# Performance work log

Measured on AMD Instinct MI355X. Metric: run time of the kernel, lower is better.

## Reference

```python
import math
import jax, jax.numpy as jnp
import numpy as np

B, T, H, A, F = 2, 2048, 2048, 2048, 8192
L, LID, EPS = 24, 0, 1e-5
NEG_INF = -1e38


def setup_inputs() -> dict:
    key = jax.random.key(0)
    ks = jax.random.split(key, 8)
    s = 0.02
    # RWKV init-derived time parameters for layer_id=0, num_hidden_layers=24
    ratio_0_to_1 = LID / (L - 1)          # 0.0
    ratio_1_to_almost_0 = 1.0 - LID / L    # 1.0
    x = jnp.arange(H, dtype=jnp.float32) / H
    tmk = jnp.power(x, ratio_1_to_almost_0)
    tmv = tmk + 0.3 * ratio_0_to_1
    tmr = jnp.power(x, 0.5 * ratio_1_to_almost_0)
    zigzag = 0.5 * (jnp.arange(1, A + 1, dtype=jnp.float32) % 3 - 1)
    time_first = jnp.full((A,), math.log(0.3), dtype=jnp.float32) + zigzag
    h = jnp.arange(A, dtype=jnp.float32)
    time_decay = -5.0 + 8.0 * (h / (A - 1)) ** (0.7 + 1.3 * ratio_0_to_1)
    return {
        'hidden': jax.random.normal(ks[0], (B, T, H), jnp.float32),
        'pre_w': jnp.ones((H,), jnp.float32), 'pre_b': jnp.zeros((H,), jnp.float32),
        'ln1_w': jnp.ones((H,), jnp.float32), 'ln1_b': jnp.zeros((H,), jnp.float32),
        'ln2_w': jnp.ones((H,), jnp.float32), 'ln2_b': jnp.zeros((H,), jnp.float32),
        'time_decay': time_decay, 'time_first': time_first,
        'tmk': tmk, 'tmv': tmv, 'tmr': tmr,
        'Wk': jax.random.normal(ks[1], (H, A), jnp.float32) * s,
        'Wv': jax.random.normal(ks[2], (H, A), jnp.float32) * s,
        'Wr': jax.random.normal(ks[3], (H, A), jnp.float32) * s,
        'Wo': jax.random.normal(ks[4], (A, H), jnp.float32) * s,
        'f_tmk': jnp.power(x, ratio_1_to_almost_0), 'f_tmr': jnp.power(x, ratio_1_to_almost_0),
        'f_Wk': jax.random.normal(ks[5], (H, F), jnp.float32) * s,
        'f_Wr': jax.random.normal(ks[6], (H, H), jnp.float32) * s,
        'f_Wv': jax.random.normal(ks[7], (F, H), jnp.float32) * s,
    }


def _ln(x, w, b):
    mu = x.mean(-1, keepdims=True)
    var = ((x - mu) ** 2).mean(-1, keepdims=True)
    return (x - mu) * jax.lax.rsqrt(var + EPS) * w + b


def _token_shift(x):
    # sx state is zeros at init: prepend a zero row, drop the last token
    return jnp.concatenate((jnp.zeros_like(x[:, :1, :]), x[:, :-1, :]), axis=1)


def _forward(hidden, pre_w, pre_b, ln1_w, ln1_b, ln2_w, ln2_b,
             time_decay, time_first, tmk, tmv, tmr, Wk, Wv, Wr, Wo,
             f_tmk, f_tmr, f_Wk, f_Wr, f_Wv):
    h0 = _ln(hidden, pre_w, pre_b)          # pre_ln (layer_id == 0)
    # ---- time mixing (RwkvSelfAttention) ----
    x1 = _ln(h0, ln1_w, ln1_b)
    cx = _token_shift(x1)
    kx = x1 * tmk + cx * (1 - tmk)
    vx = x1 * tmv + cx * (1 - tmv)
    rx = x1 * tmr + cx * (1 - tmr)
    r = jax.nn.sigmoid(rx @ Wr)             # [B,T,A]
    k = kx @ Wk
    v = vx @ Wv
    w_decay = -jnp.exp(time_decay)          # [A]

    def step(carry, kv):
        aa, bb, pp = carry                  # each [B,A]
        kk, vv = kv                         # each [B,A]
        ww = time_first + kk
        q = jnp.maximum(pp, ww)
        e1 = jnp.exp(pp - q)
        e2 = jnp.exp(ww - q)
        out = (e1 * aa + e2 * vv) / (e1 * bb + e2)
        ww2 = w_decay + pp
        q2 = jnp.maximum(ww2, kk)
        e1 = jnp.exp(ww2 - q2)
        e2 = jnp.exp(kk - q2)
        return (e1 * aa + e2 * vv, e1 * bb + e2, q2), out

    init = (jnp.zeros((B, A), k.dtype), jnp.zeros((B, A), k.dtype),
            jnp.full((B, A), NEG_INF, jnp.float32))
    _, wkv = jax.lax.scan(step, init, (jnp.swapaxes(k, 0, 1), jnp.swapaxes(v, 0, 1)))
    wkv = jnp.swapaxes(wkv, 0, 1)           # [B,T,A]
    h1 = h0 + (r * wkv) @ Wo
    # ---- channel mixing (RwkvFeedForward) ----
    x2 = _ln(h1, ln2_w, ln2_b)
    cx2 = _token_shift(x2)
    kx2 = x2 * f_tmk + cx2 * (1 - f_tmk)
    rx2 = x2 * f_tmr + cx2 * (1 - f_tmr)
    r2 = jax.nn.sigmoid(rx2 @ f_Wr)
    kk2 = jnp.square(jax.nn.relu(kx2 @ f_Wk))
    return h1 + r2 * (kk2 @ f_Wv)


def reference(hidden, pre_w, pre_b, ln1_w, ln1_b, ln2_w, ln2_b,
              time_decay, time_first, tmk, tmv, tmr, Wk, Wv, Wr, Wo,
              f_tmk, f_tmr, f_Wk, f_Wr, f_Wv):
    return _forward(hidden, pre_w, pre_b, ln1_w, ln1_b, ln2_w, ln2_b,
                    time_decay, time_first, tmk, tmv, tmr, Wk, Wv, Wr, Wo,
                    f_tmk, f_tmr, f_Wk, f_Wr, f_Wv)
```

## Files before the change

### kernel.cpp

```cpp
#include <hip/hip_runtime.h>

#define B_  2
#define T_  2048
#define H_  2048
#define A_  2048
#define F_  8192
#define BT_ 4096

typedef __bf16  bf16x8 __attribute__((ext_vector_type(8)));
typedef float   f32x4  __attribute__((ext_vector_type(4)));
typedef short   short8 __attribute__((ext_vector_type(8)));

__device__ __forceinline__ float bf2f(unsigned short b) {
  return __uint_as_float(((unsigned)b) << 16);
}
__device__ __forceinline__ unsigned short f2bf(float f) {
  unsigned u = __float_as_uint(f);
  unsigned r = (u + 0x7FFFu + ((u >> 16) & 1u)) >> 16;
  return (unsigned short)r;
}

typedef __attribute__((address_space(3))) void lds_void_t;
typedef __attribute__((address_space(1))) const void gc_void_t;
__device__ __forceinline__ void gload_lds16(const void* g, void* l) {
  __builtin_amdgcn_global_load_lds((gc_void_t*)g, (lds_void_t*)l, 16, 0, 0);
}

__global__ void canary_kernel(float* out) { out[threadIdx.x] = 1000.0f; }

__global__ __launch_bounds__(256) void transpose_bf16_kernel(
    const float* __restrict__ src, unsigned short* __restrict__ dst, int Kd, int Nd)
{
  __shared__ float tile[32][33];
  const int tx = threadIdx.x & 31;
  const int ty = threadIdx.x >> 5;
  const int n0 = blockIdx.x * 32;
  const int k0 = blockIdx.y * 32;
#pragma unroll
  for (int i = 0; i < 32; i += 8)
    tile[ty + i][tx] = src[(size_t)(k0 + ty + i) * Nd + n0 + tx];
  __syncthreads();
#pragma unroll
  for (int i = 0; i < 32; i += 8)
    dst[(size_t)(n0 + ty + i) * Kd + k0 + tx] = f2bf(tile[tx][ty + i]);
}

__device__ __forceinline__ void block_reduce2(float& a, float& b) {
#pragma unroll
  for (int off = 32; off > 0; off >>= 1) {
    a += __shfl_down(a, off, 64);
    b += __shfl_down(b, off, 64);
  }
  __shared__ float sa[4], sb[4];
  const int lane = threadIdx.x & 63, w = threadIdx.x >> 6;
  __syncthreads();
  if (lane == 0) { sa[w] = a; sb[w] = b; }
  __syncthreads();
  a = sa[0] + sa[1] + sa[2] + sa[3];
  b = sb[0] + sb[1] + sb[2] + sb[3];
}

__global__ __launch_bounds__(256) void ln_pre_kernel(
    const float* __restrict__ hidden,
    const float* __restrict__ pw, const float* __restrict__ pb,
    const float* __restrict__ w1, const float* __restrict__ b1,
    float* __restrict__ h0, unsigned short* __restrict__ x1)
{
  const int row = blockIdx.x, tid = threadIdx.x;
  const int c0 = tid * 8;
  const size_t base = (size_t)row * H_ + c0;
  float x[8];
  float4 v0 = *(const float4*)(hidden + base);
  float4 v1 = *(const float4*)(hidden + base + 4);
  x[0]=v0.x; x[1]=v0.y; x[2]=v0.z; x[3]=v0.w;
  x[4]=v1.x; x[5]=v1.y; x[6]=v1.z; x[7]=v1.w;
  float s = 0.f, s2 = 0.f;
#pragma unroll
  for (int j = 0; j < 8; ++j) { s += x[j]; s2 += x[j]*x[j]; }
  block_reduce2(s, s2);
  float mu  = s * (1.f / H_);
  float inv = rsqrtf(fmaxf(s2 * (1.f / H_) - mu*mu, 0.f) + 1e-5f);
  float y[8];
#pragma unroll
  for (int j = 0; j < 8; ++j) y[j] = (x[j] - mu) * inv * pw[c0+j] + pb[c0+j];
  *(float4*)(h0 + base)     = make_float4(y[0],y[1],y[2],y[3]);
  *(float4*)(h0 + base + 4) = make_float4(y[4],y[5],y[6],y[7]);
  s = 0.f; s2 = 0.f;
#pragma unroll
  for (int j = 0; j < 8; ++j) { s += y[j]; s2 += y[j]*y[j]; }
  block_reduce2(s, s2);
  mu  = s * (1.f / H_);
  inv = rsqrtf(fmaxf(s2 * (1.f / H_) - mu*mu, 0.f) + 1e-5f);
  unsigned o[4];
#pragma unroll
  for (int p = 0; p < 4; ++p) {
    unsigned lo = f2bf((y[2*p]   - mu) * inv * w1[c0+2*p]   + b1[c0+2*p]);
    unsigned hi = f2bf((y[2*p+1] - mu) * inv * w1[c0+2*p+1] + b1[c0+2*p+1]);
    o[p] = lo | (hi << 16);
  }
  *(uint4*)(x1 + base) = make_uint4(o[0], o[1], o[2], o[3]);
}

__global__ __launch_bounds__(256) void lnmix2_kernel(
    const float* __restrict__ h1,
    const float* __restrict__ w_, const float* __restrict__ b_,
    const float* __restrict__ tmk_, const float* __restrict__ tmr_,
    unsigned short* __restrict__ kx2b, unsigned short* __restrict__ rx2b)
{
  const int row = blockIdx.x, tid = threadIdx.x;
  const int t = row & (T_ - 1);
  const int c0 = tid * 8;
  const size_t base = (size_t)row * H_ + c0;
  float x[8], p[8];
  {
    float4 v0 = *(const float4*)(h1 + base);
    float4 v1 = *(const float4*)(h1 + base + 4);
    x[0]=v0.x; x[1]=v0.y; x[2]=v0.z; x[3]=v0.w;
    x[4]=v1.x; x[5]=v1.y; x[6]=v1.z; x[7]=v1.w;
  }
  const bool hasp = (t > 0);
  if (hasp) {
    float4 v0 = *(const float4*)(h1 + base - H_);
    float4 v1 = *(const float4*)(h1 + base - H_ + 4);
    p[0]=v0.x; p[1]=v0.y; p[2]=v0.z; p[3]=v0.w;
    p[4]=v1.x; p[5]=v1.y; p[6]=v1.z; p[7]=v1.w;
  } else {
#pragma unroll
    for (int j = 0; j < 8; ++j) p[j] = 0.f;
  }
  float s = 0.f, s2 = 0.f;
#pragma unroll
  for (int j = 0; j < 8; ++j) { s += x[j]; s2 += x[j]*x[j]; }
  block_reduce2(s, s2);
  const float mu  = s * (1.f / H_);
  const float inv = rsqrtf(fmaxf(s2 * (1.f / H_) - mu*mu, 0.f) + 1e-5f);
  float sp = 0.f, sp2 = 0.f;
#pragma unroll
  for (int j = 0; j < 8; ++j) { sp += p[j]; sp2 += p[j]*p[j]; }
  block_reduce2(sp, sp2);
  const float mup  = sp * (1.f / H_);
  const float invp = rsqrtf(fmaxf(sp2 * (1.f / H_) - mup*mup, 0.f) + 1e-5f);
  unsigned ok[4], orr[4];
#pragma unroll
  for (int q = 0; q < 4; ++q) {
    unsigned ko = 0, ro = 0;
#pragma unroll
    for (int h = 0; h < 2; ++h) {
      const int j = q*2 + h;
      const float xr = (x[j] - mu) * inv * w_[c0+j] + b_[c0+j];
      const float cr = hasp ? (p[j] - mup) * invp * w_[c0+j] + b_[c0+j] : 0.f;
      ko |= (unsigned)f2bf(fmaf(xr - cr, tmk_[c0+j], cr)) << (h*16);
      ro |= (unsigned)f2bf(fmaf(xr - cr, tmr_[c0+j], cr)) << (h*16);
    }
    ok[q] = ko; orr[q] = ro;
  }
  *(uint4*)(kx2b + base) = make_uint4(ok[0],ok[1],ok[2],ok[3]);
  *(uint4*)(rx2b + base) = make_uint4(orr[0],orr[1],orr[2],orr[3]);
}

__global__ __launch_bounds__(256) void mix1_kernel(
    const unsigned short* __restrict__ x,
    const float* __restrict__ tm_,
    unsigned short* __restrict__ outb)
{
  const int row = blockIdx.x;
  const int t = row & (T_ - 1);
  const int c0 = threadIdx.x * 8;
  const size_t base = (size_t)row * H_ + c0;
  uint4 xv = *(const uint4*)(x + base);
  uint4 cv = make_uint4(0u,0u,0u,0u);
  if (t > 0) cv = *(const uint4*)(x + base - H_);
  const unsigned xs[4] = {xv.x, xv.y, xv.z, xv.w};
  const unsigned cs[4] = {cv.x, cv.y, cv.z, cv.w};
  unsigned oo[4];
#pragma unroll
  for (int p = 0; p < 4; ++p) {
    unsigned w = 0;
#pragma unroll
    for (int h = 0; h < 2; ++h) {
      const int j = p*2 + h;
      float xf = bf2f((unsigned short)((xs[p] >> (h*16)) & 0xFFFFu));
      float cf = bf2f((unsigned short)((cs[p] >> (h*16)) & 0xFFFFu));
      w |= (unsigned)f2bf(fmaf(xf - cf, tm_[c0+j], cf)) << (h*16);
    }
    oo[p] = w;
  }
  *(uint4*)(outb + base) = make_uint4(oo[0],oo[1],oo[2],oo[3]);
}

#define WKV_G 32
#define WKV_C 32
#define WKV_L 64

__global__ __launch_bounds__(1024) void wkv_scan_kernel(
    const unsigned short* __restrict__ kg, const unsigned short* __restrict__ vg,
    const unsigned short* __restrict__ rg,
    const float* __restrict__ time_first, const float* __restrict__ time_decay,
    unsigned short* __restrict__ rwkv)
{
  const int tid = threadIdx.x;
  const int al  = tid & (WKV_G - 1);
  const int c   = tid >> 5;
  const int b   = blockIdx.x >> 6;
  const int ag  = blockIdx.x & 63;
  const int a   = ag * WKV_G + al;
  const float tf = time_first[a];
  const float w  = -__expf(time_decay[a]);
  const size_t cb = (size_t)b * T_ * A_ + a + (size_t)c * WKV_L * A_;

  float aa = 0.f, bb = 0.f, pp = -1e38f;
  {
    float kb[4], vb[4];
#pragma unroll
    for (int j = 0; j < 4; ++j) {
      kb[j] = bf2f(kg[cb + (size_t)j * A_]);
      vb[j] = bf2f(vg[cb + (size_t)j * A_]);
    }
    for (int t0 = 0; t0 < WKV_L; t0 += 4) {
#pragma unroll
      for (int j = 0; j < 4; ++j) {
        const float kk = kb[j], vv = vb[j];
        const int tn = t0 + j + 4;
        if (tn < WKV_L) {
          kb[j] = bf2f(kg[cb + (size_t)tn * A_]);
          vb[j] = bf2f(vg[cb + (size_t)tn * A_]);
        }
        float ww2 = w + pp;
        float q2  = fmaxf(ww2, kk);
        float e1  = __expf(ww2 - q2);
        float e2  = __expf(kk  - q2);
        aa = e1*aa + e2*vv;
        bb = e1*bb + e2;
        pp = q2;
      }
    }
  }
  __shared__ float saa[WKV_C][WKV_G], sbb[WKV_C][WKV_G], spp[WKV_C][WKV_G];
  saa[c][al] = aa; sbb[c][al] = bb; spp[c][al] = pp;
  __syncthreads();

  if (tid < WKV_G) {
    float Aa = 0.f, Bb = 0.f, Pp = -1e38f;
    const float Lw = (float)WKV_L * w;
    for (int cc = 0; cc < WKV_C; ++cc) {
      const float na = saa[cc][tid], nb = sbb[cc][tid], np = spp[cc][tid];
      saa[cc][tid] = Aa; sbb[cc][tid] = Bb; spp[cc][tid] = Pp;
      const float p1 = Pp + Lw;
      const float pc = fmaxf(p1, np);
      const float f1 = __expf(p1 - pc);
      const float f2 = __expf(np - pc);
      Aa = f1*Aa + f2*na;
      Bb = f1*Bb + f2*nb;
      Pp = pc;
    }
  }
  __syncthreads();
  aa = saa[c][al]; bb = sbb[c][al]; pp = spp[c][al];

  {
    float kb[4], vb[4], rb[4];
#pragma unroll
    for (int j = 0; j < 4; ++j) {
      kb[j] = bf2f(kg[cb + (size_t)j * A_]);
      vb[j] = bf2f(vg[cb + (size_t)j * A_]);
      rb[j] = bf2f(rg[cb + (size_t)j * A_]);
    }
    for (int t0 = 0; t0 < WKV_L; t0 += 4) {
#pragma unroll
      for (int j = 0; j < 4; ++j) {
        const float kk = kb[j], vv = vb[j], rr = rb[j];
        const int tn = t0 + j + 4;
        if (tn < WKV_L) {
          kb[j] = bf2f(kg[cb + (size_t)tn * A_]);
          vb[j] = bf2f(vg[cb + (size_t)tn * A_]);
          rb[j] = bf2f(rg[cb + (size_t)tn * A_]);
        }
        float ww = tf + kk;
        float q  = fmaxf(pp, ww);
        float e1 = __expf(pp - q);
        float e2 = __expf(ww - q);
        float o  = (e1*aa + e2*vv) / (e1*bb + e2);
        float sr = 1.f / (1.f + __expf(-rr));
        rwkv[cb + (size_t)(t0 + j) * A_] = f2bf(sr * o);
        float ww2 = w + pp;
        float q2  = fmaxf(ww2, kk);
        e1 = __expf(ww2 - q2);
        e2 = __expf(kk  - q2);
        aa = e1*aa + e2*vv;
        bb = e1*bb + e2;
        pp = q2;
      }
    }
  }
}

enum { EPI_BF16 = 0, EPI_ADDIP = 1, EPI_RELU2 = 2, EPI_SIGADD = 3 };

template <int BM, int NBUF, int RG, int CG, int EPI>
__global__ __launch_bounds__(512) void gemm4_kernel(
    const unsigned short* __restrict__ Ap, const unsigned short* __restrict__ Bp,
    void* __restrict__ Cp, int K, int Nn,
    const unsigned short* __restrict__ sigb)
{
  constexpr int BN = 256;
  constexpr int FM = BM / 32;
  constexpr int FN = 4;
  __shared__ unsigned short As[NBUF * BM * 64];
  __shared__ unsigned short Bs[NBUF * BN * 64];
  const int tid  = threadIdx.x;
  const int lane = tid & 63;
  const int lr = lane & 15;
  const int hi = lane >> 4;
  const int rx7 = lr & 7;
  const int wid = tid >> 6;
  const int wm = wid >> 2, wn = wid & 3;
  const int rowW = wm * (BM / 2);
  const int colW = wn * 64;
  const int gx = gridDim.x;
  const int gy = gridDim.y;
  const int flat = blockIdx.y * gx + blockIdx.x;
  const int xcd = flat & 7;
  const int j = flat >> 3;
  const int rgc = gy / RG;
  const int r_idx = xcd % rgc;
  const int c_idx = xcd / rgc;
  const int row_l = j % RG;
  const int col_l = j / RG;
  const long row0 = (long)(r_idx * RG + row_l) * BM;
  const long col0 = (long)(c_idx * CG + col_l) * BN;
  const unsigned short* Ab = Ap + (size_t)row0 * K;
  const unsigned short* Bb = Bp + (size_t)col0 * K;
  const int srow8 = tid >> 3;
  const int sslot = (tid & 7) ^ (srow8 & 7);
  f32x4 acc[FM][FN] = {};

  auto SP0 = [&](int bufi, int tt) {
    unsigned short* asb = As + bufi * (BM * 64);
    unsigned short* bsb = Bs + bufi * (BN * 64);
    const size_t ko = (size_t)tt * 64 + sslot * 8;
    gload_lds16(Ab + (size_t)srow8        * K + ko, asb + tid * 8);
    gload_lds16(Ab + (size_t)(srow8 + 64) * K + ko, asb + 4096 + tid * 8);
    gload_lds16(Bb + (size_t)srow8        * K + ko, bsb + tid * 8);
  };
  auto SP1 = [&](int bufi, int tt) {
    unsigned short* bsb = Bs + bufi * (BN * 64);
    const size_t ko = (size_t)tt * 64 + sslot * 8;
    gload_lds16(Bb + (size_t)(srow8 + 64)  * K + ko, bsb + 4096  + tid * 8);
    gload_lds16(Bb + (size_t)(srow8 + 128) * K + ko, bsb + 8192  + tid * 8);
    gload_lds16(Bb + (size_t)(srow8 + 192) * K + ko, bsb + 12288 + tid * 8);
  };
  auto SPq = [&](int bufi, int tt, int q) {
    const size_t ko = (size_t)tt * 64 + sslot * 8;
    if (q < 2) {
      unsigned short* asb = As + bufi * (BM * 64);
      gload_lds16(Ab + (size_t)(srow8 + q*128)      * K + ko, asb + q*8192 + tid * 8);
      gload_lds16(Ab + (size_t)(srow8 + q*128 + 64) * K + ko, asb + q*8192 + 4096 + tid * 8);
    } else {
      const int qq = q - 2;
      unsigned short* bsb = Bs + bufi * (BN * 64);
      gload_lds16(Bb + (size_t)(srow8 + qq*128)      * K + ko, bsb + qq*8192 + tid * 8);
      gload_lds16(Bb + (size_t)(srow8 + qq*128 + 64) * K + ko, bsb + qq*8192 + 4096 + tid * 8);
    }
  };

  const int nt = K >> 6;
  if constexpr (BM == 128) {
    SP0(0, 0); SP1(0, 0);
    if constexpr (NBUF == 3) { SP0(1, 1); SP1(1, 1); }
  } else {
#pragma unroll
    for (int q = 0; q < 4; ++q) SPq(0, 0, q);
  }
  int cur = 0;
  for (int t = 0; t < nt; ++t) {
    if constexpr (NBUF == 3) {
      if (t + 1 < nt) asm volatile("s_waitcnt vmcnt(6)" ::: "memory");
      else            asm volatile("s_waitcnt vmcnt(0)" ::: "memory");
    } else {
      asm volatile("s_waitcnt vmcnt(0)" ::: "memory");
    }
    __builtin_amdgcn_s_barrier();
    int nb = cur + (NBUF - 1); if (nb >= NBUF) nb -= NBUF;
    const unsigned short* asb = As + cur * (BM * 64);
    const unsigned short* bsb = Bs + cur * (BN * 64);
    if constexpr (BM == 128) {
#pragma unroll
      for (int kk = 0; kk < 2; ++kk) {
        bf16x8 af[4], bfr[4];
#pragma unroll
        for (int m = 0; m < 4; ++m) {
          const int row = rowW + m*16 + lr;
          const int ps = (kk*4 + hi) ^ rx7;
          af[m] = __builtin_bit_cast(bf16x8, *(const short8*)(asb + row*64 + ps*8));
        }
#pragma unroll
        for (int n = 0; n < 4; ++n) {
          const int row = colW + n*16 + lr;
          const int ps = (kk*4 + hi) ^ rx7;
          bfr[n] = __builtin_bit_cast(bf16x8, *(const short8*)(bsb + row*64 + ps*8));
        }
        if (t + NBUF - 1 < nt) { if (kk == 0) SP0(nb, t + NBUF - 1); else SP1(nb, t + NBUF - 1); }
        asm volatile("s_waitcnt lgkmcnt(0)" ::: "memory");
        __builtin_amdgcn_sched_barrier(0);
        __builtin_amdgcn_s_setprio(1);
#pragma unroll
        for (int m = 0; m < 4; ++m)
#pragma unroll
          for (int n = 0; n < 4; ++n)
            acc[m][n] = __builtin_amdgcn_mfma_f32_16x16x32_bf16(af[m], bfr[n], acc[m][n], 0, 0, 0);
        __builtin_amdgcn_s_setprio(0);
      }
    } else {
      bf16x8 bfrk[4];
#pragma unroll
      for (int sub = 0; sub < 4; ++sub) {
        const int kk = sub >> 1, mh = sub & 1;
        bf16x8 af[4];
#pragma unroll
        for (int m = 0; m < 4; ++m) {
          const int row = rowW + (mh*4 + m)*16 + lr;
          const int ps = (kk*4 + hi) ^ rx7;
          af[m] = __builtin_bit_cast(bf16x8, *(const short8*)(asb + row*64 + ps*8));
        }
        if (mh == 0) {
#pragma unroll
          for (int n = 0; n < 4; ++n) {
            const int row = colW + n*16 + lr;
            const int ps = (kk*4 + hi) ^ rx7;
            bfrk[n] = __builtin_bit_cast(bf16x8, *(const short8*)(bsb + row*64 + ps*8));
          }
        }
        if (t + 1 < nt) SPq(nb, t + 1, sub);
        asm volatile("s_waitcnt lgkmcnt(0)" ::: "memory");
        __builtin_amdgcn_sched_barrier(0);
        __builtin_amdgcn_s_setprio(1);
#pragma unroll
        for (int m = 0; m < 4; ++m)
#pragma unroll
          for (int n = 0; n < 4; ++n)
            acc[mh*4 + m][n] = __builtin_amdgcn_mfma_f32_16x16x32_bf16(af[m], bfrk[n], acc[mh*4 + m][n], 0, 0, 0);
        __builtin_amdgcn_s_setprio(0);
      }
    }
    cur = (cur + 1 == NBUF) ? 0 : cur + 1;
  }

#pragma unroll
  for (int m = 0; m < FM; ++m) {
#pragma unroll
    for (int n = 0; n < FN; ++n) {
      const long col = col0 + colW + n*16 + lr;
#pragma unroll
      for (int j2 = 0; j2 < 4; ++j2) {
        const long row = row0 + rowW + m*16 + hi*4 + j2;
        const size_t idx = (size_t)row * Nn + col;
        const float v = acc[m][n][j2];
        if (EPI == EPI_BF16) {
          ((unsigned short*)Cp)[idx] = f2bf(v);
        } else if (EPI == EPI_ADDIP) {
          float* C = (float*)Cp;
          C[idx] = C[idx] + v;
        } else if (EPI == EPI_RELU2) {
          float rr = v > 0.f ? v : 0.f;
          ((unsigned short*)Cp)[idx] = f2bf(rr * rr);
        } else {
          float s = 1.f / (1.f + __expf(-bf2f(sigb[idx])));
          float* C = (float*)Cp;
          C[idx] = C[idx] + s * v;
        }
      }
    }
  }
}

#define MB(x) ((size_t)(x) << 20)
#define WS_NEED MB(184)

extern "C" void kernel_launch(void* const* d_in, const int* in_sizes, int n_in,
                              void* d_out, int out_size, void* d_ws, size_t ws_size,
                              hipStream_t stream) {
  const float* hidden     = (const float*)d_in[0];
  const float* pre_w      = (const float*)d_in[1];
  const float* pre_b      = (const float*)d_in[2];
  const float* ln1_w      = (const float*)d_in[3];
  const float* ln1_b      = (const float*)d_in[4];
  const float* ln2_w      = (const float*)d_in[5];
  const float* ln2_b      = (const float*)d_in[6];
  const float* time_decay = (const float*)d_in[7];
  const float* time_first = (const float*)d_in[8];
  const float* tmk        = (const float*)d_in[9];
  const float* tmv        = (const float*)d_in[10];
  const float* tmr        = (const float*)d_in[11];
  const float* Wk         = (const float*)d_in[12];
  const float* Wv         = (const float*)d_in[13];
  const float* Wr         = (const float*)d_in[14];
  const float* Wo         = (const float*)d_in[15];
  const float* f_tmk      = (const float*)d_in[16];
  const float* f_tmr      = (const float*)d_in[17];
  const float* f_Wk       = (const float*)d_in[18];
  const float* f_Wr       = (const float*)d_in[19];
  const float* f_Wv       = (const float*)d_in[20];
  float* out = (float*)d_out;
  char*  ws  = (char*)d_ws;

  if (ws_size < WS_NEED) {
    canary_kernel<<<1, 256, 0, stream>>>(out);
    return;
  }

  unsigned short* fWkT = (unsigned short*)(ws + MB(0));
  unsigned short* fWvT = (unsigned short*)(ws + MB(32));
  unsigned short* WkT  = (unsigned short*)(ws + MB(64));
  unsigned short* WvT  = (unsigned short*)(ws + MB(72));
  unsigned short* WrT  = (unsigned short*)(ws + MB(80));
  unsigned short* WoT  = (unsigned short*)(ws + MB(88));
  unsigned short* fWrT = (unsigned short*)(ws + MB(96));
  unsigned short* KK   = (unsigned short*)(ws + MB(64));
  unsigned short* S1   = (unsigned short*)(ws + MB(104));
  unsigned short* S4   = (unsigned short*)(ws + MB(120));
  unsigned short* S2   = (unsigned short*)(ws + MB(136));
  unsigned short* S3   = (unsigned short*)(ws + MB(152));
  unsigned short* M1   = (unsigned short*)(ws + MB(168));

  const dim3 blk(256);
  const dim3 blk512(512);
  const dim3 gSmall(8, 32);
  const dim3 gRelu(32, 16);

  transpose_bf16_kernel<<<dim3(64, 64),  blk, 0, stream>>>(Wk,   WkT,  2048, 2048);
  transpose_bf16_kernel<<<dim3(64, 64),  blk, 0, stream>>>(Wv,   WvT,  2048, 2048);
  transpose_bf16_kernel<<<dim3(64, 64),  blk, 0, stream>>>(Wr,   WrT,  2048, 2048);
  transpose_bf16_kernel<<<dim3(64, 64),  blk, 0, stream>>>(Wo,   WoT,  2048, 2048);
  transpose_bf16_kernel<<<dim3(64, 64),  blk, 0, stream>>>(f_Wr, fWrT, 2048, 2048);
  transpose_bf16_kernel<<<dim3(256, 64), blk, 0, stream>>>(f_Wk, fWkT, 2048, 8192);
  transpose_bf16_kernel<<<dim3(64, 256), blk, 0, stream>>>(f_Wv, fWvT, 8192, 2048);

  ln_pre_kernel<<<BT_, blk, 0, stream>>>(hidden, pre_w, pre_b, ln1_w, ln1_b, out, S1);

  mix1_kernel<<<BT_, blk, 0, stream>>>(S1, tmk, M1);
  gemm4_kernel<128,3,8,4,EPI_BF16><<<gSmall, blk512, 0, stream>>>(M1, WkT, S2, 2048, 2048, nullptr);
  mix1_kernel<<<BT_, blk, 0, stream>>>(S1, tmv, M1);
  gemm4_kernel<128,3,8,4,EPI_BF16><<<gSmall, blk512, 0, stream>>>(M1, WvT, S3, 2048, 2048, nullptr);
  mix1_kernel<<<BT_, blk, 0, stream>>>(S1, tmr, M1);
  gemm4_kernel<128,3,8,4,EPI_BF16><<<gSmall, blk512, 0, stream>>>(M1, WrT, S4, 2048, 2048, nullptr);

  wkv_scan_kernel<<<dim3(128), dim3(1024), 0, stream>>>(S2, S3, S4, time_first, time_decay, S1);

  gemm4_kernel<128,3,8,4,EPI_ADDIP><<<gSmall, blk512, 0, stream>>>(S1, WoT, out, 2048, 2048, nullptr);

  lnmix2_kernel<<<BT_, blk, 0, stream>>>(out, ln2_w, ln2_b, f_tmk, f_tmr, M1, S2);

  gemm4_kernel<128,3,8,4,EPI_BF16><<<gSmall, blk512, 0, stream>>>(S2, fWrT, S3, 2048, 2048, nullptr);

  gemm4_kernel<256,2,8,8,EPI_RELU2><<<gRelu, blk512, 0, stream>>>(M1, fWkT, KK, 2048, 8192, nullptr);

  gemm4_kernel<128,3,8,4,EPI_SIGADD><<<gSmall, blk512, 0, stream>>>(KK, fWvT, out, 8192, 2048, S3);
}
```

Baseline: 703.6 us.

## Rework GEMM pipeline into double-buffered K-half stages with finer-grained prefetch

Replaces the 3-buffer (and 2-buffer for BM=256) GEMM mainloop with a double buffer. Each 64-wide K tile is split into two 32-wide halves, each with its own barrier and prefetch slot. The LDS layout changes to 32-element rows with a 4-way XOR swizzle. This cuts LDS use, which may allow more occupancy, and aims to overlap loads at half-tile granularity. It adds an extra barrier per tile and a different bank-conflict pattern.

```diff
diff --git a/kernel.cpp b/kernel.cpp
--- a/kernel.cpp
+++ b/kernel.cpp
@@ -296,8 +296,8 @@
 
 enum { EPI_BF16 = 0, EPI_ADDIP = 1, EPI_RELU2 = 2, EPI_SIGADD = 3 };
 
-template <int BM, int NBUF, int RG, int CG, int EPI>
-__global__ __launch_bounds__(512) void gemm4_kernel(
+template <int BM, int RG, int CG, int EPI>
+__global__ __launch_bounds__(512) void gemm5_kernel(
     const unsigned short* __restrict__ Ap, const unsigned short* __restrict__ Bp,
     void* __restrict__ Cp, int K, int Nn,
     const unsigned short* __restrict__ sigb)
@@ -305,13 +305,13 @@
   constexpr int BN = 256;
   constexpr int FM = BM / 32;
   constexpr int FN = 4;
-  __shared__ unsigned short As[NBUF * BM * 64];
-  __shared__ unsigned short Bs[NBUF * BN * 64];
+  __shared__ unsigned short As[2 * BM * 64];
+  __shared__ unsigned short Bs[2 * BN * 64];
   const int tid  = threadIdx.x;
   const int lane = tid & 63;
   const int lr = lane & 15;
   const int hi = lane >> 4;
-  const int rx7 = lr & 7;
+  const int ps8 = (hi ^ (lr & 3)) * 8;
   const int wid = tid >> 6;
   const int wm = wid >> 2, wn = wid & 3;
   const int rowW = wm * (BM / 2);
@@ -330,107 +330,72 @@
   const long col0 = (long)(c_idx * CG + col_l) * BN;
   const unsigned short* Ab = Ap + (size_t)row0 * K;
   const unsigned short* Bb = Bp + (size_t)col0 * K;
-  const int srow8 = tid >> 3;
-  const int sslot = (tid & 7) ^ (srow8 & 7);
+  const int srow4 = tid >> 2;
+  const int sslot4 = (tid & 3) ^ (srow4 & 3);
   f32x4 acc[FM][FN] = {};
 
-  auto SP0 = [&](int bufi, int tt) {
-    unsigned short* asb = As + bufi * (BM * 64);
-    unsigned short* bsb = Bs + bufi * (BN * 64);
-    const size_t ko = (size_t)tt * 64 + sslot * 8;
-    gload_lds16(Ab + (size_t)srow8        * K + ko, asb + tid * 8);
-    gload_lds16(Ab + (size_t)(srow8 + 64) * K + ko, asb + 4096 + tid * 8);
-    gload_lds16(Bb + (size_t)srow8        * K + ko, bsb + tid * 8);
+  auto SP = [&](int bufi, int tt, int kh) {
+    const size_t ko = (size_t)tt * 64 + kh * 32 + sslot4 * 8;
+    unsigned short* asb = As + bufi * (BM * 64) + kh * (BM * 32);
+    unsigned short* bsb = Bs + bufi * (BN * 64) + kh * (BN * 32);
+    if constexpr (BM == 128) {
+      gload_lds16(Ab + (size_t)srow4 * K + ko, asb + tid * 8);
+    } else {
+      gload_lds16(Ab + (size_t)srow4         * K + ko, asb + tid * 8);
+      gload_lds16(Ab + (size_t)(srow4 + 128) * K + ko, asb + 4096 + tid * 8);
+    }
+    gload_lds16(Bb + (size_t)srow4         * K + ko, bsb + tid * 8);
+    gload_lds16(Bb + (size_t)(srow4 + 128) * K + ko, bsb + 4096 + tid * 8);
   };
-  auto SP1 = [&](int bufi, int tt) {
-    unsigned short* bsb = Bs + bufi * (BN * 64);
-    const size_t ko = (size_t)tt * 64 + sslot * 8;
-    gload_lds16(Bb + (size_t)(srow8 + 64)  * K + ko, bsb + 4096  + tid * 8);
-    gload_lds16(Bb + (size_t)(srow8 + 128) * K + ko, bsb + 8192  + tid * 8);
-    gload_lds16(Bb + (size_t)(srow8 + 192) * K + ko, bsb + 12288 + tid * 8);
-  };
-  auto SPq = [&](int bufi, int tt, int q) {
-    const size_t ko = (size_t)tt * 64 + sslot * 8;
-    if (q < 2) {
-      unsigned short* asb = As + bufi * (BM * 64);
-      gload_lds16(Ab + (size_t)(srow8 + q*128)      * K + ko, asb + q*8192 + tid * 8);
-      gload_lds16(Ab + (size_t)(srow8 + q*128 + 64) * K + ko, asb + q*8192 + 4096 + tid * 8);
-    } else {
-      const int qq = q - 2;
-      unsigned short* bsb = Bs + bufi * (BN * 64);
-      gload_lds16(Bb + (size_t)(srow8 + qq*128)      * K + ko, bsb + qq*8192 + tid * 8);
-      gload_lds16(Bb + (size_t)(srow8 + qq*128 + 64) * K + ko, bsb + qq*8192 + 4096 + tid * 8);
-    }
-  };
 
   const int nt = K >> 6;
-  if constexpr (BM == 128) {
-    SP0(0, 0); SP1(0, 0);
-    if constexpr (NBUF == 3) { SP0(1, 1); SP1(1, 1); }
-  } else {
-#pragma unroll
-    for (int q = 0; q < 4; ++q) SPq(0, 0, q);
-  }
-  int cur = 0;
+  SP(0, 0, 0); SP(0, 0, 1); SP(1, 1, 0);
   for (int t = 0; t < nt; ++t) {
-    if constexpr (NBUF == 3) {
-      if (t + 1 < nt) asm volatile("s_waitcnt vmcnt(6)" ::: "memory");
-      else            asm volatile("s_waitcnt vmcnt(0)" ::: "memory");
-    } else {
-      asm volatile("s_waitcnt vmcnt(0)" ::: "memory");
-    }
-    __builtin_amdgcn_s_barrier();
-    int nb = cur + (NBUF - 1); if (nb >= NBUF) nb -= NBUF;
+    const int cur = t & 1;
     const unsigned short* asb = As + cur * (BM * 64);
     const unsigned short* bsb = Bs + cur * (BN * 64);
+    const bool c1 = (t + 1 < nt);
     if constexpr (BM == 128) {
-#pragma unroll
-      for (int kk = 0; kk < 2; ++kk) {
-        bf16x8 af[4], bfr[4];
-#pragma unroll
-        for (int m = 0; m < 4; ++m) {
-          const int row = rowW + m*16 + lr;
-          const int ps = (kk*4 + hi) ^ rx7;
-          af[m] = __builtin_bit_cast(bf16x8, *(const short8*)(asb + row*64 + ps*8));
-        }
-#pragma unroll
-        for (int n = 0; n < 4; ++n) {
-          const int row = colW + n*16 + lr;
-          const int ps = (kk*4 + hi) ^ rx7;
-          bfr[n] = __builtin_bit_cast(bf16x8, *(const short8*)(bsb + row*64 + ps*8));
-        }
-        if (t + NBUF - 1 < nt) { if (kk == 0) SP0(nb, t + NBUF - 1); else SP1(nb, t + NBUF - 1); }
-        asm volatile("s_waitcnt lgkmcnt(0)" ::: "memory");
-        __builtin_amdgcn_sched_barrier(0);
-        __builtin_amdgcn_s_setprio(1);
-#pragma unroll
-        for (int m = 0; m < 4; ++m)
-#pragma unroll
-          for (int n = 0; n < 4; ++n)
-            acc[m][n] = __builtin_amdgcn_mfma_f32_16x16x32_bf16(af[m], bfr[n], acc[m][n], 0, 0, 0);
-        __builtin_amdgcn_s_setprio(0);
-      }
+      if (c1) asm volatile("s_waitcnt vmcnt(6)" ::: "memory");
+      else    asm volatile("s_waitcnt vmcnt(3)" ::: "memory");
+    } else {
+      if (c1) asm volatile("s_waitcnt vmcnt(8)" ::: "memory");
+      else    asm volatile("s_waitcnt vmcnt(4)" ::: "memory");
+    }
+    __builtin_amdgcn_s_barrier();
+    if (c1) SP((t + 1) & 1, t + 1, 1);
+    if constexpr (BM == 128) {
+      bf16x8 af[4], bfr[4];
+#pragma unroll
+      for (int m = 0; m < 4; ++m)
+        af[m] = __builtin_bit_cast(bf16x8,
+            *(const short8*)(asb + (rowW + m*16 + lr) * 32 + ps8));
+#pragma unroll
+      for (int n = 0; n < 4; ++n)
+        bfr[n] = __builtin_bit_cast(bf16x8,
+            *(const short8*)(bsb + (colW + n*16 + lr) * 32 + ps8));
+      asm volatile("s_waitcnt lgkmcnt(0)" ::: "memory");
+      __builtin_amdgcn_sched_barrier(0);
+      __builtin_amdgcn_s_setprio(1);
+#pragma unroll
+      for (int m = 0; m < 4; ++m)
+#pragma unroll
+        for (int n = 0; n < 4; ++n)
+          acc[m][n] = __builtin_amdgcn_mfma_f32_16x16x32_bf16(af[m], bfr[n], acc[m][n], 0, 0, 0);
+      __builtin_amdgcn_s_setprio(0);
     } else {
       bf16x8 bfrk[4];
 #pragma unroll
-      for (int sub = 0; sub < 4; ++sub) {
-        const int kk = sub >> 1, mh = sub & 1;
+      for (int n = 0; n < 4; ++n)
+        bfrk[n] = __builtin_bit_cast(bf16x8,
+            *(const short8*)(bsb + (colW + n*16 + lr) * 32 + ps8));
+#pragma unroll
+      for (int mh = 0; mh < 2; ++mh) {
         bf16x8 af[4];
 #pragma unroll
-        for (int m = 0; m < 4; ++m) {
-          const int row = rowW + (mh*4 + m)*16 + lr;
-          const int ps = (kk*4 + hi) ^ rx7;
-          af[m] = __builtin_bit_cast(bf16x8, *(const short8*)(asb + row*64 + ps*8));
-        }
-        if (mh == 0) {
-#pragma unroll
-          for (int n = 0; n < 4; ++n) {
-            const int row = colW + n*16 + lr;
-            const int ps = (kk*4 + hi) ^ rx7;
-            bfrk[n] = __builtin_bit_cast(bf16x8, *(const short8*)(bsb + row*64 + ps*8));
-          }
-        }
-        if (t + 1 < nt) SPq(nb, t + 1, sub);
+        for (int m = 0; m < 4; ++m)
+          af[m] = __builtin_bit_cast(bf16x8,
+              *(const short8*)(asb + (rowW + (mh*4 + m)*16 + lr) * 32 + ps8));
         asm volatile("s_waitcnt lgkmcnt(0)" ::: "memory");
         __builtin_amdgcn_sched_barrier(0);
         __builtin_amdgcn_s_setprio(1);
@@ -442,7 +407,62 @@
         __builtin_amdgcn_s_setprio(0);
       }
     }
-    cur = (cur + 1 == NBUF) ? 0 : cur + 1;
+    if constexpr (BM == 128) {
+      if (c1) asm volatile("s_waitcnt vmcnt(6)" ::: "memory");
+      else    asm volatile("s_waitcnt vmcnt(0)" ::: "memory");
+    } else {
+      if (c1) asm volatile("s_waitcnt vmcnt(8)" ::: "memory");
+      else    asm volatile("s_waitcnt vmcnt(0)" ::: "memory");
+    }
+    __builtin_amdgcn_s_barrier();
+    if (t + 2 < nt) SP(cur, t + 2, 0);
+    {
+      const unsigned short* asb1 = asb + BM * 32;
+      const unsigned short* bsb1 = bsb + BN * 32;
+      if constexpr (BM == 128) {
+        bf16x8 af[4], bfr[4];
+#pragma unroll
+        for (int m = 0; m < 4; ++m)
+          af[m] = __builtin_bit_cast(bf16x8,
+              *(const short8*)(asb1 + (rowW + m*16 + lr) * 32 + ps8));
+#pragma unroll
+        for (int n = 0; n < 4; ++n)
+          bfr[n] = __builtin_bit_cast(bf16x8,
+              *(const short8*)(bsb1 + (colW + n*16 + lr) * 32 + ps8));
+        asm volatile("s_waitcnt lgkmcnt(0)" ::: "memory");
+        __builtin_amdgcn_sched_barrier(0);
+        __builtin_amdgcn_s_setprio(1);
+#pragma unroll
+        for (int m = 0; m < 4; ++m)
+#pragma unroll
+          for (int n = 0; n < 4; ++n)
+            acc[m][n] = __builtin_amdgcn_mfma_f32_16x16x32_bf16(af[m], bfr[n], acc[m][n], 0, 0, 0);
+        __builtin_amdgcn_s_setprio(0);
+      } else {
+        bf16x8 bfrk[4];
+#pragma unroll
+        for (int n = 0; n < 4; ++n)
+          bfrk[n] = __builtin_bit_cast(bf16x8,
+              *(const short8*)(bsb1 + (colW + n*16 + lr) * 32 + ps8));
+#pragma unroll
+        for (int mh = 0; mh < 2; ++mh) {
+          bf16x8 af[4];
+#pragma unroll
+          for (int m = 0; m < 4; ++m)
+            af[m] = __builtin_bit_cast(bf16x8,
+                *(const short8*)(asb1 + (rowW + (mh*4 + m)*16 + lr) * 32 + ps8));
+          asm volatile("s_waitcnt lgkmcnt(0)" ::: "memory");
+          __builtin_amdgcn_sched_barrier(0);
+          __builtin_amdgcn_s_setprio(1);
+#pragma unroll
+          for (int m = 0; m < 4; ++m)
+#pragma unroll
+            for (int n = 0; n < 4; ++n)
+              acc[mh*4 + m][n] = __builtin_amdgcn_mfma_f32_16x16x32_bf16(af[m], bfrk[n], acc[mh*4 + m][n], 0, 0, 0);
+          __builtin_amdgcn_s_setprio(0);
+        }
+      }
+    }
   }
 
 #pragma unroll
@@ -538,21 +558,21 @@
   ln_pre_kernel<<<BT_, blk, 0, stream>>>(hidden, pre_w, pre_b, ln1_w, ln1_b, out, S1);
 
   mix1_kernel<<<BT_, blk, 0, stream>>>(S1, tmk, M1);
-  gemm4_kernel<128,3,8,4,EPI_BF16><<<gSmall, blk512, 0, stream>>>(M1, WkT, S2, 2048, 2048, nullptr);
+  gemm5_kernel<128,8,4,EPI_BF16><<<gSmall, blk512, 0, stream>>>(M1, WkT, S2, 2048, 2048, nullptr);
   mix1_kernel<<<BT_, blk, 0, stream>>>(S1, tmv, M1);
-  gemm4_kernel<128,3,8,4,EPI_BF16><<<gSmall, blk512, 0, stream>>>(M1, WvT, S3, 2048, 2048, nullptr);
+  gemm5_kernel<128,8,4,EPI_BF16><<<gSmall, blk512, 0, stream>>>(M1, WvT, S3, 2048, 2048, nullptr);
   mix1_kernel<<<BT_, blk, 0, stream>>>(S1, tmr, M1);
-  gemm4_kernel<128,3,8,4,EPI_BF16><<<gSmall, blk512, 0, stream>>>(M1, WrT, S4, 2048, 2048, nullptr);
+  gemm5_kernel<128,8,4,EPI_BF16><<<gSmall, blk512, 0, stream>>>(M1, WrT, S4, 2048, 2048, nullptr);
 
   wkv_scan_kernel<<<dim3(128), dim3(1024), 0, stream>>>(S2, S3, S4, time_first, time_decay, S1);
 
-  gemm4_kernel<128,3,8,4,EPI_ADDIP><<<gSmall, blk512, 0, stream>>>(S1, WoT, out, 2048, 2048, nullptr);
+  gemm5_kernel<128,8,4,EPI_ADDIP><<<gSmall, blk512, 0, stream>>>(S1, WoT, out, 2048, 2048, nullptr);
 
   lnmix2_kernel<<<BT_, blk, 0, stream>>>(out, ln2_w, ln2_b, f_tmk, f_tmr, M1, S2);
 
-  gemm4_kernel<128,3,8,4,EPI_BF16><<<gSmall, blk512, 0, stream>>>(S2, fWrT, S3, 2048, 2048, nullptr);
-
-  gemm4_kernel<256,2,8,8,EPI_RELU2><<<gRelu, blk512, 0, stream>>>(M1, fWkT, KK, 2048, 8192, nullptr);
-
-  gemm4_kernel<128,3,8,4,EPI_SIGADD><<<gSmall, blk512, 0, stream>>>(KK, fWvT, out, 8192, 2048, S3);
-}
+  gemm5_kernel<128,8,4,EPI_BF16><<<gSmall, blk512, 0, stream>>>(S2, fWrT, S3, 2048, 2048, nullptr);
+
+  gemm5_kernel<256,8,8,EPI_RELU2><<<gRelu, blk512, 0, stream>>>(M1, fWkT, KK, 2048, 8192, nullptr);
+
+  gemm5_kernel<128,8,4,EPI_SIGADD><<<gSmall, blk512, 0, stream>>>(KK, fWvT, out, 8192, 2048, S3);
+}
```

New measurement: 940.6 us. 33.7% more time.
